# Kernel tuning notes

Measured on AMD Instinct MI355X. Metric: run time of the kernel, lower is better.

Reference implementation:

```python
import jax, jax.numpy as jnp
import numpy as np

B, T, D = 2, 1024, 1024
C = 16384
K_GT = 8
TOPK = 16
BLOCK = 8192
TF_ALPHA = 0.5  # teacher_force_alpha: soft mix of GT and predicted features


def setup_inputs() -> dict:
    key = jax.random.key(0)
    k1, k2, k3, k4 = jax.random.split(key, 4)
    hidden = jax.random.normal(k1, (B, T, D), dtype=jnp.float32)
    # Linear(n_embd, n_concepts_padded, bias=False) -> weight (C, D)
    predictor_w = jax.random.normal(k2, (C, D), dtype=jnp.float32) * 0.02
    # Embedding(n_concepts_padded, concept_dim)
    concept_emb = jax.random.normal(k3, (C, D), dtype=jnp.float32) * 0.02
    concept_ids = jax.random.randint(k4, (B, T, K_GT), 0, C, dtype=jnp.int32)
    concept_mask = jnp.ones((B, T, K_GT), dtype=bool)
    return {
        "hidden": hidden,
        "predictor_w": predictor_w,
        "concept_emb": concept_emb,
        "concept_ids": concept_ids,
        "concept_mask": concept_mask,
    }


def _streaming_topk(hidden, predictor_w):
    """Block-wise top-k over concept logits, never materializing (B,T,C).
    Returns topk_logits (B,T,TOPK), topk_indices (B,T,TOPK)."""
    n_blocks = C // BLOCK
    w_blocks = predictor_w.reshape(n_blocks, BLOCK, D)
    offsets = jnp.arange(n_blocks, dtype=jnp.int32) * BLOCK

    def step(carry, inp):
        top_l, top_i = carry  # (B,T,TOPK)
        w_blk, off = inp
        logits = jnp.einsum("btd,cd->btc", hidden, w_blk)  # (B,T,BLOCK)
        blk_idx = off + jnp.arange(BLOCK, dtype=jnp.int32)
        cand_l = jnp.concatenate([top_l, logits], axis=-1)
        cand_i = jnp.concatenate(
            [top_i, jnp.broadcast_to(blk_idx, logits.shape)], axis=-1
        )
        new_l, pos = jax.lax.top_k(cand_l, TOPK)
        new_i = jnp.take_along_axis(cand_i, pos, axis=-1)
        return (new_l, new_i), None

    init = (
        jnp.full((B, T, TOPK), -jnp.inf, dtype=hidden.dtype),
        jnp.zeros((B, T, TOPK), dtype=jnp.int32),
    )
    (top_l, top_i), _ = jax.lax.scan(step, init, (w_blocks, offsets))
    return top_l, top_i


def reference(hidden, predictor_w, concept_emb, concept_ids, concept_mask):
    # ---- predicted features via streaming top-k (sparse weighted embedding sum)
    topk_logits, topk_idx = _streaming_topk(hidden, predictor_w)
    weights = jax.nn.sigmoid(topk_logits)  # (B,T,TOPK); topk_on_logits=False is
    # equivalent since sigmoid is monotone
    topk_emb = concept_emb[topk_idx]  # (B,T,TOPK,D) gather
    predicted = jnp.einsum("btk,btkd->btd", weights, topk_emb)

    # ---- ground-truth pooled features (scatter-add over valid concept ids)
    valid = concept_mask & (concept_ids != -1)  # (B,T,K)
    safe_ids = jnp.where(valid, concept_ids, 0)
    gt_emb = concept_emb[safe_ids] * valid[..., None].astype(concept_emb.dtype)
    gt_features = gt_emb.sum(axis=2)  # (B,T,D)

    # ---- soft teacher forcing mix
    features = TF_ALPHA * gt_features + (1.0 - TF_ALPHA) * predicted
    return features
```

## Files before the change

kernel.cpp:

```cpp
#include <hip/hip_runtime.h>
#include <math.h>

#define B_    2
#define T_    1024
#define D_    1024
#define C_    16384
#define KGT   8
#define TOPK  16
#define ROWS  (B_*T_)

#define NSPLIT 16
#define CS     (C_/NSPLIT)
#define NC     (NSPLIT*TOPK)
#define NREF   32

#define RT_A   64
#define CAND   512
#define THRESH 1.4f

typedef __bf16 bf16x8 __attribute__((ext_vector_type(8)));
typedef float  f32x4  __attribute__((ext_vector_type(4)));

#define BAR_CHUNK() do { \
    asm volatile("s_waitcnt vmcnt(0)\n\ts_barrier" ::: "memory"); \
    __builtin_amdgcn_sched_barrier(0); } while (0)

__device__ __forceinline__ unsigned short bf16_rne(float x) {
    unsigned int u = __float_as_uint(x);
    unsigned int r = (u + 0x7FFFu + ((u >> 16) & 1u)) >> 16;
    return (unsigned short)r;
}

__device__ __forceinline__ void pack_hi_one(const float* __restrict__ src,
                                            uint4* __restrict__ dhi, size_t gt)
{
    int lane = (int)(gt & 63);
    size_t f = gt >> 6;
    int ks = (int)(f & 31);
    size_t rf = f >> 5;
    size_t row = rf * 16 + (lane & 15);
    int k0 = ks * 32 + (lane >> 4) * 8;
    const float4* s = (const float4*)(src + row * D_ + k0);
    float4 x0 = s[0], x1 = s[1];
    float v[8] = {x0.x, x0.y, x0.z, x0.w, x1.x, x1.y, x1.z, x1.w};
    unsigned short h[8];
    #pragma unroll
    for (int i = 0; i < 8; ++i) h[i] = bf16_rne(v[i]);
    uint4 ph;
    ph.x = h[0] | ((unsigned)h[1] << 16); ph.y = h[2] | ((unsigned)h[3] << 16);
    ph.z = h[4] | ((unsigned)h[5] << 16); ph.w = h[6] | ((unsigned)h[7] << 16);
    dhi[f * 64 + lane] = ph;
}

#define NWPACK ((C_/16)*32*64/256)

__global__ __launch_bounds__(256)
void pack_hi_all_kernel(const float* __restrict__ W, const float* __restrict__ hidden,
                        uint4* __restrict__ Wh, uint4* __restrict__ Ah)
{
    int bid = blockIdx.x;
    if (bid < NWPACK) {
        pack_hi_one(W, Wh, (size_t)bid * 256 + threadIdx.x);
    } else {
        pack_hi_one(hidden, Ah, (size_t)(bid - NWPACK) * 256 + threadIdx.x);
    }
}

__global__ __launch_bounds__(256)
void zero_cnt_kernel(unsigned* __restrict__ cnt)
{
    cnt[blockIdx.x * 256 + threadIdx.x] = 0u;
}

#define ASTAGE(cc_) do {                                                          \
    const int ccS = (cc_);                                                        \
    const int kc0 = (ccS & 3) * 8;                                                \
    uint4* dstb = &Abuf[(ccS & 1)*2048];                                          \
    _Pragma("unroll")                                                             \
    for (int t = 0; t < 4; ++t) {                                                 \
        int s = t*8 + w;                                                          \
        int kci = s >> 2, ai = s & 3;                                             \
        const uint4* srcp = Ah + ((size_t)((rb*4 + ai)*32 + kc0 + kci))*64 + lane;\
        __builtin_amdgcn_global_load_lds(                                         \
            (const __attribute__((address_space(1))) void*)srcp,                  \
            (__attribute__((address_space(3))) void*)&dstb[s*64],                 \
            16, 0, 0);                                                            \
    } } while (0)

__global__ __launch_bounds__(512, 4)
void mfma_logits_thresh_kernel(const uint4* __restrict__ Wh, const uint4* __restrict__ Ah,
                               float* __restrict__ candVal, unsigned short* __restrict__ candIdx,
                               unsigned* __restrict__ cnt)
{
    __shared__ uint4 Abuf[4096];

    const int tid  = threadIdx.x;
    const int lane = tid & 63;
    const int w    = tid >> 6;
    const int d    = blockIdx.x;
    const int rb   = (d >> 3) & 31;
    const int sp   = ((d & 7) << 1) | (d >> 8);

    const uint4* Wwave = Wh + ((size_t)(sp*64 + w*2) * 32) * 64 + lane;

    const int rloc = (lane >> 4) * 4;
    const int cloc = lane & 15;

    f32x4 acc[4][2];

    ASTAGE(0);

    #pragma unroll 1
    for (int cc = 0; cc < 16; ++cc) {
        const int ct = cc >> 2;
        const int ch = cc & 3;

        BAR_CHUNK();
        if (cc + 1 < 16) ASTAGE(cc + 1);

        if (ch == 0) {
            #pragma unroll
            for (int i = 0; i < 4; ++i)
                #pragma unroll
                for (int j = 0; j < 2; ++j)
                    acc[i][j] = (f32x4){0.f, 0.f, 0.f, 0.f};
        }

        const uint4* abuf = &Abuf[(cc & 1)*2048];
        const uint4* wch  = Wwave + ((size_t)(ct*16)*32 + ch*8)*64;
        #pragma unroll
        for (int kci = 0; kci < 8; ++kci) {
            bf16x8 a[4], b[2];
            #pragma unroll
            for (int i = 0; i < 4; ++i)
                a[i] = *(const bf16x8*)&abuf[(kci*4 + i)*64 + lane];
            #pragma unroll
            for (int j = 0; j < 2; ++j)
                b[j] = *(const bf16x8*)&wch[((size_t)j*32 + kci)*64];
            #pragma unroll
            for (int j = 0; j < 2; ++j)
                #pragma unroll
                for (int i = 0; i < 4; ++i)
                    acc[i][j] = __builtin_amdgcn_mfma_f32_16x16x32_bf16(
                        a[i], b[j], acc[i][j], 0, 0, 0);
        }

        if (ch == 3) {
            #pragma unroll
            for (int j = 0; j < 2; ++j) {
                const int gc = sp*1024 + (ct*16 + w*2 + j)*16 + cloc;
                #pragma unroll
                for (int i = 0; i < 4; ++i)
                    #pragma unroll
                    for (int jj = 0; jj < 4; ++jj) {
                        float v = acc[i][j][jj];
                        if (v > THRESH) {
                            int grow = rb*RT_A + i*16 + rloc + jj;
                            unsigned slot = atomicAdd(&cnt[grow], 1u);
                            if (slot < CAND) {
                                candVal[(size_t)grow*CAND + slot] = v;
                                candIdx[(size_t)grow*CAND + slot] = (unsigned short)gc;
                            }
                        }
                    }
            }
        }
    }
}

__global__ __launch_bounds__(256, 4)
void concept_finalize_kernel(const float* __restrict__ hidden,
                             const float* __restrict__ W,
                             const float* __restrict__ emb,
                             const int* __restrict__ ids,
                             const float* __restrict__ candVal,
                             const unsigned short* __restrict__ candIdx,
                             const unsigned* __restrict__ cnt,
                             float* __restrict__ out)
{
    __shared__ float  cv[CAND];
    __shared__ int    ciL[CAND];
    __shared__ int    slot32[NREF];
    __shared__ double refv[NREF];
    __shared__ float  selW[TOPK];
    __shared__ int    selIdx[TOPK];

    const int tid = threadIdx.x;
    const int row = blockIdx.x;

    int n = (int)cnt[row];
    if (n > CAND) n = CAND;

    #pragma unroll
    for (int h = 0; h < 2; ++h) {
        int s = tid + h*256;
        cv[s]  = (s < n) ? candVal[(size_t)row*CAND + s] : -INFINITY;
        ciL[s] = (s < n) ? (int)candIdx[(size_t)row*CAND + s] : 0;
    }
    if (tid < NREF) slot32[tid] = -1;
    __syncthreads();

    #pragma unroll
    for (int h = 0; h < 2; ++h) {
        int s = tid + h*256;
        if (s < n) {
            float v = cv[s]; int rank = 0;
            for (int j = 0; j < n; ++j) {
                float u = cv[j];
                rank += (u > v) || ((u == v) && (j < s));
            }
            if (rank < NREF) slot32[rank] = s;
        }
    }
    __syncthreads();

    {
        const int g = tid >> 3, l = tid & 7;
        const int s = slot32[g];
        const int c = (s >= 0) ? ciL[s] : 0;
        const float4* W4 = (const float4*)W;
        const float4* H4 = (const float4*)hidden;
        double acc = 0.0;
        #pragma unroll 4
        for (int q = 0; q < 32; ++q) {
            float4 wv = W4[(size_t)c*(D_/4) + q*8 + l];
            float4 hv = H4[(size_t)row*(D_/4) + q*8 + l];
            acc += (double)hv.x*(double)wv.x + (double)hv.y*(double)wv.y
                 + (double)hv.z*(double)wv.z + (double)hv.w*(double)wv.w;
        }
        acc += __shfl_xor(acc, 1);
        acc += __shfl_xor(acc, 2);
        acc += __shfl_xor(acc, 4);
        if (l == 0) refv[g] = (s >= 0) ? acc : -1.0e300;
    }
    __syncthreads();

    if (tid < NREF) {
        double v = refv[tid]; int rank = 0;
        for (int j = 0; j < NREF; ++j) {
            double u = refv[j];
            rank += (u > v) || ((u == v) && (j < tid));
        }
        if (rank < TOPK) {
            selIdx[rank] = (slot32[tid] >= 0) ? ciL[slot32[tid]] : 0;
            selW[rank]   = 1.0f / (1.0f + expf(-(float)v));
        }
    }
    __syncthreads();

    const float4* E4 = (const float4*)emb;
    float px = 0.f, py = 0.f, pz = 0.f, pw = 0.f;
    #pragma unroll
    for (int k = 0; k < TOPK; ++k) {
        float wt = selW[k];
        float4 e = E4[(size_t)selIdx[k]*(D_/4) + tid];
        px = fmaf(wt, e.x, px); py = fmaf(wt, e.y, py);
        pz = fmaf(wt, e.z, pz); pw = fmaf(wt, e.w, pw);
    }
    float gx = 0.f, gy = 0.f, gz = 0.f, gw = 0.f;
    #pragma unroll
    for (int k = 0; k < KGT; ++k) {
        int c = ids[row*KGT + k];
        float4 e = E4[(size_t)c*(D_/4) + tid];
        gx += e.x; gy += e.y; gz += e.z; gw += e.w;
    }
    float4 o;
    o.x = 0.5f*(gx + px); o.y = 0.5f*(gy + py);
    o.z = 0.5f*(gz + pz); o.w = 0.5f*(gw + pw);
    ((float4*)out)[(size_t)row*(D_/4) + tid] = o;
}

#define RT     64
#define CT     256
#define KC     16
#define HP4    5
#define LTP    65

__global__ __launch_bounds__(256, 2)
void concept_logits_topk_kernel(const float* __restrict__ hidden,
                                const float* __restrict__ W,
                                float* __restrict__ candVal,
                                unsigned short* __restrict__ candIdx)
{
    __shared__ float4 uni[1040];
    __shared__ float4 hT[RT * HP4];
    __shared__ float tval[TOPK * 256];
    __shared__ unsigned short tidx[TOPK * 256];

    float* ltile = (float*)uni;

    const int tid  = threadIdx.x;
    const int row0 = blockIdx.x * RT;
    const int cs0  = blockIdx.y * CS;
    const float4* H4 = (const float4*)hidden;
    const float4* W4 = (const float4*)W;

    #pragma unroll
    for (int e = 0; e < TOPK; ++e) tval[e*256 + tid] = -INFINITY;
    float minval = -INFINITY;
    int   minpos = 0;

    const int rg   = tid >> 5;
    const int cg   = tid & 31;
    const int srow = tid >> 2;
    const int ssub = tid & 3;

    for (int ct = 0; ct < CS/CT; ++ct) {
        const int cbase = cs0 + ct*CT;
        float acc[8][8];
        #pragma unroll
        for (int i = 0; i < 8; ++i)
            #pragma unroll
            for (int j = 0; j < 8; ++j) acc[i][j] = 0.f;

        for (int kc = 0; kc < D_/KC; ++kc) {
            __syncthreads();
            #pragma unroll
            for (int i = 0; i < 4; ++i) {
                int idx = i*256 + tid;
                int wr = idx >> 2, c4 = idx & 3;
                uni[c4*CT + wr] = W4[(size_t)(cbase + wr)*(D_/4) + kc*(KC/4) + c4];
            }
            {
                int hr = tid >> 2, c4 = tid & 3;
                hT[hr*HP4 + c4] = H4[(size_t)(row0 + hr)*(D_/4) + kc*(KC/4) + c4];
            }
            __syncthreads();
            #pragma unroll
            for (int k4 = 0; k4 < KC/4; ++k4) {
                float4 a[8];
                #pragma unroll
                for (int i = 0; i < 8; ++i) a[i] = hT[(rg*8 + i)*HP4 + k4];
                #pragma unroll
                for (int j = 0; j < 8; ++j) {
                    float4 wv = uni[k4*CT + (j*32 + cg)];
                    #pragma unroll
                    for (int i = 0; i < 8; ++i) {
                        acc[i][j] = fmaf(a[i].x, wv.x, acc[i][j]);
                        acc[i][j] = fmaf(a[i].y, wv.y, acc[i][j]);
                        acc[i][j] = fmaf(a[i].z, wv.z, acc[i][j]);
                        acc[i][j] = fmaf(a[i].w, wv.w, acc[i][j]);
                    }
                }
            }
        }

        #pragma unroll
        for (int q = 0; q < 4; ++q) {
            __syncthreads();
            #pragma unroll
            for (int i = 0; i < 8; ++i) {
                #pragma unroll
                for (int jj = 0; jj < 2; ++jj) {
                    int ci = q*2 + jj;
                    ltile[(rg*8 + i)*LTP + (jj*32 + cg)] = acc[i][ci];
                }
            }
            __syncthreads();
            #pragma unroll
            for (int i = 0; i < 16; ++i) {
                float v = ltile[srow*LTP + ssub*16 + i];
                if (v > minval) {
                    int gc = cbase + q*64 + ssub*16 + i;
                    tval[minpos*256 + tid] = v;
                    tidx[minpos*256 + tid] = (unsigned short)gc;
                    minval = INFINITY;
                    #pragma unroll
                    for (int e = 0; e < TOPK; ++e) {
                        float tv_ = tval[e*256 + tid];
                        if (tv_ < minval) { minval = tv_; minpos = e; }
                    }
                }
            }
        }
    }
    __syncthreads();

    if (tid < RT) {
        const int rr = tid;
        float* cvp = candVal + (size_t)(row0 + rr)*NC + blockIdx.y*TOPK;
        unsigned short* cip = candIdx + (size_t)(row0 + rr)*NC + blockIdx.y*TOPK;
        for (int k = 0; k < TOPK; ++k) {
            float best = -INFINITY; int bp = 0;
            for (int s = 0; s < 4; ++s) {
                int col = rr*4 + s;
                #pragma unroll
                for (int e = 0; e < TOPK; ++e) {
                    float v = tval[e*256 + col];
                    if (v > best) { best = v; bp = e*256 + col; }
                }
            }
            cvp[k] = best;
            cip[k] = tidx[bp];
            tval[bp] = -INFINITY;
        }
    }
}

__global__ __launch_bounds__(256, 4)
void concept_finalize256_kernel(const float* __restrict__ hidden,
                                const float* __restrict__ W,
                                const float* __restrict__ emb,
                                const int* __restrict__ ids,
                                const float* __restrict__ candVal,
                                const unsigned short* __restrict__ candIdx,
                                float* __restrict__ out)
{
    __shared__ float  cval[NC];
    __shared__ int    cidx[NC];
    __shared__ int    slot[NREF];
    __shared__ double refv[NREF];
    __shared__ float  selW[TOPK];
    __shared__ int    selIdx[TOPK];

    const int tid = threadIdx.x;
    const int row = blockIdx.x;

    cval[tid] = candVal[(size_t)row*NC + tid];
    cidx[tid] = (int)candIdx[(size_t)row*NC + tid];
    __syncthreads();

    {
        float v = cval[tid]; int rank = 0;
        for (int j = 0; j < NC; ++j) {
            float u = cval[j];
            rank += (u > v) || ((u == v) && (j < tid));
        }
        if (rank < NREF) slot[rank] = tid;
    }
    __syncthreads();

    {
        const int g = tid >> 3, l = tid & 7;
        const int c = cidx[slot[g]];
        const float4* W4 = (const float4*)W;
        const float4* H4 = (const float4*)hidden;
        double acc = 0.0;
        #pragma unroll 4
        for (int s = 0; s < 32; ++s) {
            float4 wv = W4[(size_t)c*(D_/4) + s*8 + l];
            float4 hv = H4[(size_t)row*(D_/4) + s*8 + l];
            acc += (double)hv.x*(double)wv.x + (double)hv.y*(double)wv.y
                 + (double)hv.z*(double)wv.z + (double)hv.w*(double)wv.w;
        }
        acc += __shfl_xor(acc, 1);
        acc += __shfl_xor(acc, 2);
        acc += __shfl_xor(acc, 4);
        if (l == 0) refv[g] = acc;
    }
    __syncthreads();

    if (tid < NREF) {
        double v = refv[tid]; int rank = 0;
        for (int j = 0; j < NREF; ++j) {
            double u = refv[j];
            rank += (u > v) || ((u == v) && (j < tid));
        }
        if (rank < TOPK) {
            selIdx[rank] = cidx[slot[tid]];
            selW[rank]   = 1.0f / (1.0f + expf(-(float)v));
        }
    }
    __syncthreads();

    const float4* E4 = (const float4*)emb;
    float px = 0.f, py = 0.f, pz = 0.f, pw = 0.f;
    #pragma unroll
    for (int k = 0; k < TOPK; ++k) {
        float wt = selW[k];
        float4 e = E4[(size_t)selIdx[k]*(D_/4) + tid];
        px = fmaf(wt, e.x, px); py = fmaf(wt, e.y, py);
        pz = fmaf(wt, e.z, pz); pw = fmaf(wt, e.w, pw);
    }
    float gx = 0.f, gy = 0.f, gz = 0.f, gw = 0.f;
    #pragma unroll
    for (int k = 0; k < KGT; ++k) {
        int c = ids[row*KGT + k];
        float4 e = E4[(size_t)c*(D_/4) + tid];
        gx += e.x; gy += e.y; gz += e.z; gw += e.w;
    }
    float4 o;
    o.x = 0.5f*(gx + px); o.y = 0.5f*(gy + py);
    o.z = 0.5f*(gz + pz); o.w = 0.5f*(gw + pw);
    ((float4*)out)[(size_t)row*(D_/4) + tid] = o;
}

extern "C" void kernel_launch(void* const* d_in, const int* in_sizes, int n_in,
                              void* d_out, int out_size, void* d_ws, size_t ws_size,
                              hipStream_t stream)
{
    (void)in_sizes; (void)n_in; (void)out_size;
    const float* hidden = (const float*)d_in[0];
    const float* W      = (const float*)d_in[1];
    const float* emb    = (const float*)d_in[2];
    const int*   ids    = (const int*)d_in[3];
    float* out = (float*)d_out;

    const size_t szWh = (size_t)C_ * D_ * 2;
    const size_t szAh = (size_t)ROWS * D_ * 2;
    const size_t szCV = (size_t)ROWS * CAND * sizeof(float);
    const size_t szCI = (size_t)ROWS * CAND * sizeof(unsigned short);
    const size_t szCN = (size_t)ROWS * sizeof(unsigned);
    const size_t need = szWh + szAh + szCV + szCI + szCN;

    if (ws_size >= need) {
        char* p = (char*)d_ws;
        uint4* Wh = (uint4*)p;               p += szWh;
        uint4* Ah = (uint4*)p;               p += szAh;
        float* candVal = (float*)p;          p += szCV;
        unsigned short* candIdx = (unsigned short*)p;  p += szCI;
        unsigned* cnt = (unsigned*)p;

        hipLaunchKernelGGL(zero_cnt_kernel, dim3(ROWS/256), dim3(256), 0, stream, cnt);
        const int nPack = NWPACK + (ROWS/16)*32*64/256;
        hipLaunchKernelGGL(pack_hi_all_kernel, dim3(nPack), dim3(256), 0, stream,
                           W, hidden, Wh, Ah);
        hipLaunchKernelGGL(mfma_logits_thresh_kernel, dim3(512), dim3(512), 0, stream,
                           Wh, Ah, candVal, candIdx, cnt);
        hipLaunchKernelGGL(concept_finalize_kernel, dim3(ROWS), dim3(256), 0, stream,
                           hidden, W, emb, ids, candVal, candIdx, cnt, out);
    } else {
        float* candVal = (float*)d_ws;
        unsigned short* candIdx =
            (unsigned short*)((char*)d_ws + (size_t)ROWS*NC*sizeof(float));
        hipLaunchKernelGGL(concept_logits_topk_kernel, dim3(ROWS/RT, NSPLIT), dim3(256), 0, stream,
                           hidden, W, candVal, candIdx);
        hipLaunchKernelGGL(concept_finalize256_kernel, dim3(ROWS), dim3(256), 0, stream,
                           hidden, W, emb, ids, candVal, candIdx, out);
    }
}
```

Measured before the change: 215.3 us.

## Retile MFMA logits kernel to 64x512 per block and fuse counter zeroing into pack

The logits kernel now gives each block 64 rows by 512 concepts, with each wave holding a 4x4 grid of accumulator tiles. The A tile is staged once per k-chunk instead of being reloaded for every 16-column group, and the grid doubles to 1024 blocks. The separate zero-count kernel is folded into the pack kernel as extra blocks, removing one launch. The larger accumulator set raises register pressure, which may lower occupancy under the 512x4 launch bounds.

```diff
diff --git a/kernel.cpp b/kernel.cpp
--- a/kernel.cpp
+++ b/kernel.cpp
@@ -9,9 +9,9 @@
 #define TOPK  16
 #define ROWS  (B_*T_)
 
-#define NSPLIT 16
-#define CS     (C_/NSPLIT)
-#define NC     (NSPLIT*TOPK)
+#define NSPLIT32 32
+#define NC     256
+#define CS     1024
 #define NREF   32
 
 #define RT_A   64
@@ -53,29 +53,26 @@
 }
 
 #define NWPACK ((C_/16)*32*64/256)
+#define NAPACK ((ROWS/16)*32*64/256)
 
 __global__ __launch_bounds__(256)
 void pack_hi_all_kernel(const float* __restrict__ W, const float* __restrict__ hidden,
-                        uint4* __restrict__ Wh, uint4* __restrict__ Ah)
+                        uint4* __restrict__ Wh, uint4* __restrict__ Ah,
+                        unsigned* __restrict__ cnt)
 {
     int bid = blockIdx.x;
     if (bid < NWPACK) {
         pack_hi_one(W, Wh, (size_t)bid * 256 + threadIdx.x);
+    } else if (bid < NWPACK + NAPACK) {
+        pack_hi_one(hidden, Ah, (size_t)(bid - NWPACK) * 256 + threadIdx.x);
     } else {
-        pack_hi_one(hidden, Ah, (size_t)(bid - NWPACK) * 256 + threadIdx.x);
-    }
-}
-
-__global__ __launch_bounds__(256)
-void zero_cnt_kernel(unsigned* __restrict__ cnt)
-{
-    cnt[blockIdx.x * 256 + threadIdx.x] = 0u;
-}
-
-#define ASTAGE(cc_) do {                                                          \
-    const int ccS = (cc_);                                                        \
-    const int kc0 = (ccS & 3) * 8;                                                \
-    uint4* dstb = &Abuf[(ccS & 1)*2048];                                          \
+        cnt[(bid - NWPACK - NAPACK) * 256 + threadIdx.x] = 0u;
+    }
+}
+
+#define ASTAGE(c_) do {                                                           \
+    const int kc0 = (c_) * 8;                                                     \
+    uint4* dstb = &Abuf[((c_) & 1)*2048];                                         \
     _Pragma("unroll")                                                             \
     for (int t = 0; t < 4; ++t) {                                                 \
         int s = t*8 + w;                                                          \
@@ -98,73 +95,65 @@
     const int lane = tid & 63;
     const int w    = tid >> 6;
     const int d    = blockIdx.x;
-    const int rb   = (d >> 3) & 31;
-    const int sp   = ((d & 7) << 1) | (d >> 8);
-
-    const uint4* Wwave = Wh + ((size_t)(sp*64 + w*2) * 32) * 64 + lane;
-
-    const int rloc = (lane >> 4) * 4;
-    const int cloc = lane & 15;
-
-    f32x4 acc[4][2];
+    const int idx  = d >> 3;
+    const int sp   = (d & 7) * 4 + (idx >> 5);
+    const int rb   = idx & 31;
+
+    const uint4* Wwave = Wh + ((size_t)(sp*32 + w*4) * 32) * 64 + lane;
+
+    f32x4 acc[4][4];
+    #pragma unroll
+    for (int i = 0; i < 4; ++i)
+        #pragma unroll
+        for (int j = 0; j < 4; ++j)
+            acc[i][j] = (f32x4){0.f, 0.f, 0.f, 0.f};
 
     ASTAGE(0);
 
     #pragma unroll 1
-    for (int cc = 0; cc < 16; ++cc) {
-        const int ct = cc >> 2;
-        const int ch = cc & 3;
-
+    for (int c = 0; c < 4; ++c) {
         BAR_CHUNK();
-        if (cc + 1 < 16) ASTAGE(cc + 1);
-
-        if (ch == 0) {
-            #pragma unroll
-            for (int i = 0; i < 4; ++i)
-                #pragma unroll
-                for (int j = 0; j < 2; ++j)
-                    acc[i][j] = (f32x4){0.f, 0.f, 0.f, 0.f};
-        }
-
-        const uint4* abuf = &Abuf[(cc & 1)*2048];
-        const uint4* wch  = Wwave + ((size_t)(ct*16)*32 + ch*8)*64;
+        if (c + 1 < 4) ASTAGE(c + 1);
+
+        const uint4* abuf = &Abuf[(c & 1)*2048];
+        const uint4* wch  = Wwave + (size_t)(c*8)*64;
         #pragma unroll
         for (int kci = 0; kci < 8; ++kci) {
-            bf16x8 a[4], b[2];
+            bf16x8 a[4], b[4];
             #pragma unroll
             for (int i = 0; i < 4; ++i)
                 a[i] = *(const bf16x8*)&abuf[(kci*4 + i)*64 + lane];
             #pragma unroll
-            for (int j = 0; j < 2; ++j)
+            for (int j = 0; j < 4; ++j)
                 b[j] = *(const bf16x8*)&wch[((size_t)j*32 + kci)*64];
             #pragma unroll
-            for (int j = 0; j < 2; ++j)
+            for (int j = 0; j < 4; ++j)
                 #pragma unroll
                 for (int i = 0; i < 4; ++i)
                     acc[i][j] = __builtin_amdgcn_mfma_f32_16x16x32_bf16(
                         a[i], b[j], acc[i][j], 0, 0, 0);
         }
-
-        if (ch == 3) {
-            #pragma unroll
-            for (int j = 0; j < 2; ++j) {
-                const int gc = sp*1024 + (ct*16 + w*2 + j)*16 + cloc;
-                #pragma unroll
-                for (int i = 0; i < 4; ++i)
-                    #pragma unroll
-                    for (int jj = 0; jj < 4; ++jj) {
-                        float v = acc[i][j][jj];
-                        if (v > THRESH) {
-                            int grow = rb*RT_A + i*16 + rloc + jj;
-                            unsigned slot = atomicAdd(&cnt[grow], 1u);
-                            if (slot < CAND) {
-                                candVal[(size_t)grow*CAND + slot] = v;
-                                candIdx[(size_t)grow*CAND + slot] = (unsigned short)gc;
-                            }
-                        }
+    }
+
+    const int rloc = (lane >> 4) * 4;
+    const int cloc = lane & 15;
+    #pragma unroll
+    for (int j = 0; j < 4; ++j) {
+        const int gc = sp*512 + (w*4 + j)*16 + cloc;
+        #pragma unroll
+        for (int i = 0; i < 4; ++i)
+            #pragma unroll
+            for (int jj = 0; jj < 4; ++jj) {
+                float v = acc[i][j][jj];
+                if (v > THRESH) {
+                    int grow = rb*RT_A + i*16 + rloc + jj;
+                    unsigned slot = atomicAdd(&cnt[grow], 1u);
+                    if (slot < CAND) {
+                        candVal[(size_t)grow*CAND + slot] = v;
+                        candIdx[(size_t)grow*CAND + slot] = (unsigned short)gc;
                     }
-            }
-        }
+                }
+            }
     }
 }
 
@@ -511,11 +500,10 @@
         unsigned short* candIdx = (unsigned short*)p;  p += szCI;
         unsigned* cnt = (unsigned*)p;
 
-        hipLaunchKernelGGL(zero_cnt_kernel, dim3(ROWS/256), dim3(256), 0, stream, cnt);
-        const int nPack = NWPACK + (ROWS/16)*32*64/256;
+        const int nPack = NWPACK + NAPACK + ROWS/256;
         hipLaunchKernelGGL(pack_hi_all_kernel, dim3(nPack), dim3(256), 0, stream,
-                           W, hidden, Wh, Ah);
-        hipLaunchKernelGGL(mfma_logits_thresh_kernel, dim3(512), dim3(512), 0, stream,
+                           W, hidden, Wh, Ah, cnt);
+        hipLaunchKernelGGL(mfma_logits_thresh_kernel, dim3(1024), dim3(512), 0, stream,
                            Wh, Ah, candVal, candIdx, cnt);
         hipLaunchKernelGGL(concept_finalize_kernel, dim3(ROWS), dim3(256), 0, stream,
                            hidden, W, emb, ids, candVal, candIdx, cnt, out);
@@ -523,7 +511,7 @@
         float* candVal = (float*)d_ws;
         unsigned short* candIdx =
             (unsigned short*)((char*)d_ws + (size_t)ROWS*NC*sizeof(float));
-        hipLaunchKernelGGL(concept_logits_topk_kernel, dim3(ROWS/RT, NSPLIT), dim3(256), 0, stream,
+        hipLaunchKernelGGL(concept_logits_topk_kernel, dim3(ROWS/RT, C_/CS), dim3(256), 0, stream,
                            hidden, W, candVal, candIdx);
         hipLaunchKernelGGL(concept_finalize256_kernel, dim3(ROWS), dim3(256), 0, stream,
                            hidden, W, emb, ids, candVal, candIdx, out);
```

New measurement: 271.5 us. +26.1%, slower.
